# Kernel tuning notes

Hardware: AMD Instinct MI355X
Metric: run time of the kernel (lower is better)

The kernel has to match this reference:

```python
import jax, jax.numpy as jnp
import numpy as np

N = 8192        # nodes
D_IN = 512      # input features
H = 256         # hidden (GAT out_features)
D_OUT = 16      # output classes
K = 16          # num clusters/classes
LRELU_SLOPE = 0.2
MASK_FILL = -9e15
EDGE_P = 0.002  # sparsity of random adjacency


def setup_inputs() -> dict:
    key = jax.random.key(0)
    k1, k2, k3, k4, k5, k6 = jax.random.split(key, 6)
    x = jax.random.normal(k1, (N, D_IN), dtype=jnp.float32)
    # binary adjacency with self loops (module only tests adj > 0; support reused as propagation matrix)
    adj = (jax.random.uniform(k2, (N, N)) < EDGE_P).astype(jnp.float32)
    adj = jnp.maximum(adj, jnp.eye(N, dtype=jnp.float32))
    C_a = jax.random.normal(k3, (K, H), dtype=jnp.float32)
    # learned parameters (xavier-ish scale)
    W = jax.random.normal(k4, (D_IN, H), dtype=jnp.float32) * (1.414 * (2.0 / (D_IN + H)) ** 0.5)
    a = jax.random.normal(k5, (2 * H, 1), dtype=jnp.float32) * (1.414 * (2.0 / (2 * H + 1)) ** 0.5)
    W_gcn = jax.random.normal(k6, (H, D_OUT), dtype=jnp.float32)
    return {"x": x, "adj": adj, "C_a": C_a, "W": W, "a": a, "W_gcn": W_gcn}


def _clust_score(Z, C):
    # score[n,k] = exp(-||Z_n - C_k||) normalized over k (beta = 1)
    d = jnp.sqrt(((Z[:, None, :] - C[None, :, :]) ** 2).sum(-1))  # [N,K]
    s = jnp.exp(-d) + 1e-10
    return s / s.sum(axis=1, keepdims=True)


def reference(x, adj, C_a, W, a, W_gcn):
    h = W.shape[1]
    # --- GAT layer ---
    Wh = x @ W                                   # [N,H]
    Wh1 = Wh @ a[:h, :]                          # [N,1]
    Wh2 = Wh @ a[h:, :]                          # [N,1]
    e = jax.nn.leaky_relu(Wh1 + Wh2.T, LRELU_SLOPE)   # [N,N]
    att = jax.nn.softmax(jnp.where(adj > 0, e, MASK_FILL), axis=1)
    Z_0 = att @ Wh                               # h_prime, [N,H]
    gatoutput = jax.nn.elu(Z_0)
    # --- cluster score on detached Z_0 (update=False path) ---
    score = _clust_score(jax.lax.stop_gradient(Z_0), C_a)
    # --- GCN layer (B_1 = I, so Z_1 = F_1) ---
    F_1 = jax.nn.relu(adj @ (gatoutput @ W_gcn))  # [N,D_OUT]
    output = F_1
    Z_1 = F_1
    return (output, Z_1, Z_0, score)
```

## Files before the change

kernel.cpp:

```cpp
#include <hip/hip_runtime.h>
#include <hip/hip_bf16.h>

#define N_NODES 8192
#define D_IN    512
#define H       256
#define D_OUT   16
#define K_CL    16
#define MAXN    96

#define OUT_OFF 0
#define Z1_OFF  131072
#define Z0_OFF  262144
#define SC_OFF  2359296

typedef unsigned int   u32;
typedef unsigned short u16;
typedef __attribute__((ext_vector_type(8))) short bf16x8;
typedef __attribute__((ext_vector_type(4))) float f32x4;

__device__ __forceinline__ float load_in(const void* p, int bf, size_t idx) {
    if (bf) { u32 w = ((const u16*)p)[idx]; return __uint_as_float(w << 16); }
    return ((const float*)p)[idx];
}
__device__ __forceinline__ void store_out(void* p, int bf, size_t idx, float v) {
    if (bf) ((__hip_bfloat16*)p)[idx] = __float2bfloat16(v);
    else    ((float*)p)[idx] = v;
}

__global__ void k_detect(const u32* __restrict__ adjw, int* __restrict__ flag) {
    int t = blockIdx.x * 256 + threadIdx.x;
    int hit = 0;
    #pragma unroll 4
    for (int i = 0; i < 16; i++)
        if (adjw[(size_t)t + (size_t)i * 65536] == 0x00003F80u) hit = 1;
    if (hit) atomicOr(flag, 1);
}

__global__ void k_prep_small(const void* av, const void* C_a, const void* Wgcn,
                             const int* __restrict__ flag,
                             float* a_f, float* Ca_f, float* Wg_f) {
    int bf = *flag;
    int i = blockIdx.x * 256 + threadIdx.x;
    if (i < 512)        a_f[i]         = load_in(av,   bf, i);
    else if (i < 4608)  Ca_f[i - 512]  = load_in(C_a,  bf, i - 512);
    else if (i < 8704)  Wg_f[i - 4608] = load_in(Wgcn, bf, i - 4608);
}

__global__ void k_prep_wt(const void* __restrict__ wraw,
                          const int* __restrict__ flag, u16* __restrict__ Wt) {
    int bf = *flag;
    int idx = blockIdx.x * 256 + threadIdx.x;
    int h = idx >> 9, k = idx & 511;
    float v = load_in(wraw, bf, (size_t)k * H + h);
    __hip_bfloat16 b = __float2bfloat16(v);
    Wt[(size_t)h * D_IN + k] = *(u16*)&b;
}

__global__ __launch_bounds__(256) void k_gemm_wh(
    const void* __restrict__ xraw, const void* __restrict__ wraw,
    const u16* __restrict__ Wt,
    const int* __restrict__ flag, float* __restrict__ Wh)
{
    int bf = *flag;
    __shared__ float xs[32][68];
    __shared__ float ws_[32][68];
    int tid = threadIdx.x;
    int bm = blockIdx.x >> 2, bn = blockIdx.x & 3;
    int m0 = bm * 64, n0 = bn * 64;

    if (bf) {
        int wave = tid >> 6, lane = tid & 63;
        int wr = wave >> 1, wc = wave & 1;
        int r0 = m0 + wr * 32, c0 = n0 + wc * 32;
        int lr = lane & 15, lk = lane >> 4;
        const u16* xp = (const u16*)xraw;
        const u16* a0p = xp + (size_t)(r0 + lr)      * D_IN + lk * 8;
        const u16* a1p = xp + (size_t)(r0 + 16 + lr) * D_IN + lk * 8;
        const u16* b0p = Wt + (size_t)(c0 + lr)      * D_IN + lk * 8;
        const u16* b1p = Wt + (size_t)(c0 + 16 + lr) * D_IN + lk * 8;
        f32x4 acc[2][2] = {};
        #pragma unroll 4
        for (int k0 = 0; k0 < D_IN; k0 += 32) {
            bf16x8 a0 = *(const bf16x8*)(a0p + k0);
            bf16x8 a1 = *(const bf16x8*)(a1p + k0);
            bf16x8 b0 = *(const bf16x8*)(b0p + k0);
            bf16x8 b1 = *(const bf16x8*)(b1p + k0);
            acc[0][0] = __builtin_amdgcn_mfma_f32_16x16x32_bf16(a0, b0, acc[0][0], 0, 0, 0);
            acc[0][1] = __builtin_amdgcn_mfma_f32_16x16x32_bf16(a0, b1, acc[0][1], 0, 0, 0);
            acc[1][0] = __builtin_amdgcn_mfma_f32_16x16x32_bf16(a1, b0, acc[1][0], 0, 0, 0);
            acc[1][1] = __builtin_amdgcn_mfma_f32_16x16x32_bf16(a1, b1, acc[1][1], 0, 0, 0);
        }
        #pragma unroll
        for (int i = 0; i < 2; i++) {
            #pragma unroll
            for (int reg = 0; reg < 4; reg++) {
                int r = r0 + 16 * i + 4 * lk + reg;
                Wh[(size_t)r * H + c0 + lr]      = acc[i][0][reg];
                Wh[(size_t)r * H + c0 + 16 + lr] = acc[i][1][reg];
            }
        }
        return;
    }

    int tx = tid & 15, ty = tid >> 4;
    float acc[4][4] = {};
    for (int k0 = 0; k0 < D_IN; k0 += 32) {
        {
            int r = tid >> 2, kq = (tid & 3) * 8;
            size_t base = (size_t)(m0 + r) * D_IN + k0 + kq;
            float4 f0 = *(const float4*)((const float*)xraw + base);
            float4 f1 = *(const float4*)((const float*)xraw + base + 4);
            xs[kq + 0][r] = f0.x; xs[kq + 1][r] = f0.y;
            xs[kq + 2][r] = f0.z; xs[kq + 3][r] = f0.w;
            xs[kq + 4][r] = f1.x; xs[kq + 5][r] = f1.y;
            xs[kq + 6][r] = f1.z; xs[kq + 7][r] = f1.w;
        }
        {
            int kk = tid >> 3, n8 = (tid & 7) * 8;
            size_t base = (size_t)(k0 + kk) * H + n0 + n8;
            float4 f0 = *(const float4*)((const float*)wraw + base);
            float4 f1 = *(const float4*)((const float*)wraw + base + 4);
            ws_[kk][n8+0]=f0.x; ws_[kk][n8+1]=f0.y; ws_[kk][n8+2]=f0.z; ws_[kk][n8+3]=f0.w;
            ws_[kk][n8+4]=f1.x; ws_[kk][n8+5]=f1.y; ws_[kk][n8+6]=f1.z; ws_[kk][n8+7]=f1.w;
        }
        __syncthreads();
        #pragma unroll
        for (int kk = 0; kk < 32; kk++) {
            float4 a4 = *(const float4*)&xs[kk][ty * 4];
            float4 b4 = *(const float4*)&ws_[kk][tx * 4];
            float a[4] = {a4.x, a4.y, a4.z, a4.w};
            float b[4] = {b4.x, b4.y, b4.z, b4.w};
            #pragma unroll
            for (int i = 0; i < 4; i++)
                #pragma unroll
                for (int j = 0; j < 4; j++)
                    acc[i][j] += a[i] * b[j];
        }
        __syncthreads();
    }
    #pragma unroll
    for (int i = 0; i < 4; i++) {
        float4 o = {acc[i][0], acc[i][1], acc[i][2], acc[i][3]};
        *(float4*)&Wh[(size_t)(m0 + ty*4 + i) * H + n0 + tx*4] = o;
    }
}

__global__ __launch_bounds__(256) void k_wh12(
    const float* __restrict__ Wh, const float* __restrict__ a_f,
    float* __restrict__ Wh1, float* __restrict__ Wh2)
{
    int tid = threadIdx.x;
    int wave = tid >> 6, lane = tid & 63;
    int n = blockIdx.x * 4 + wave;
    float4 v  = *(const float4*)(Wh + (size_t)n * H + lane * 4);
    float4 a1 = *(const float4*)(a_f + lane * 4);
    float4 a2 = *(const float4*)(a_f + H + lane * 4);
    float s1 = v.x*a1.x + v.y*a1.y + v.z*a1.z + v.w*a1.w;
    float s2 = v.x*a2.x + v.y*a2.y + v.z*a2.z + v.w*a2.w;
    #pragma unroll
    for (int off = 32; off; off >>= 1) {
        s1 += __shfl_xor(s1, off);
        s2 += __shfl_xor(s2, off);
    }
    if (lane == 0) { Wh1[n] = s1; Wh2[n] = s2; }
}

__global__ __launch_bounds__(256) void k_gat_row(
    const void* __restrict__ adjraw, const int* __restrict__ flag,
    const float* __restrict__ Wh,
    const float* __restrict__ Wh1, const float* __restrict__ Wh2,
    const float* __restrict__ Ca_f, const float* __restrict__ Wg_f,
    float* __restrict__ Gf,
    int* __restrict__ nbr_cnt, u16* __restrict__ nbr_idx,
    void* __restrict__ dout)
{
    const int n = blockIdx.x;
    const int tid = threadIdx.x;
    const int bf = *flag;
    __shared__ int   s_cnt;
    __shared__ int   s_idx[MAXN];
    __shared__ float s_att[MAXN];
    __shared__ float s_z[H];
    __shared__ float s_g[H];
    __shared__ float s_red[256];
    __shared__ float s_sc[16];

    if (tid == 0) s_cnt = 0;
    __syncthreads();

    if (bf) {
        const u16* arow = (const u16*)adjraw + (size_t)n * N_NODES;
        #pragma unroll
        for (int it = 0; it < 4; it++) {
            int base = it * 2048 + tid * 8;
            uint4 raw = *(const uint4*)(arow + base);
            u32 rw[4] = {raw.x, raw.y, raw.z, raw.w};
            #pragma unroll
            for (int q = 0; q < 4; q++) {
                #pragma unroll
                for (int hh = 0; hh < 2; hh++) {
                    u32 u = (rw[q] >> (16 * hh)) & 0xFFFFu;
                    if (__uint_as_float(u << 16) > 0.f) {
                        int p = atomicAdd(&s_cnt, 1);
                        if (p < MAXN) s_idx[p] = base + q * 2 + hh;
                    }
                }
            }
        }
    } else {
        const float* arow = (const float*)adjraw + (size_t)n * N_NODES;
        #pragma unroll
        for (int it = 0; it < 8; it++) {
            int base = it * 1024 + tid * 4;
            float4 v = *(const float4*)(arow + base);
            float vv[4] = {v.x, v.y, v.z, v.w};
            #pragma unroll
            for (int q = 0; q < 4; q++) {
                if (vv[q] > 0.f) {
                    int p = atomicAdd(&s_cnt, 1);
                    if (p < MAXN) s_idx[p] = base + q;
                }
            }
        }
    }
    __syncthreads();
    const int cnt = min(s_cnt, MAXN);
    if (tid == 0) nbr_cnt[n] = cnt;
    if (tid < cnt) nbr_idx[(size_t)n * MAXN + tid] = (u16)s_idx[tid];

    float e = 0.f;
    if (tid < cnt) {
        float v = Wh1[n] + Wh2[s_idx[tid]];
        e = v > 0.f ? v : 0.2f * v;
    }
    int lane = tid & 63, wv = tid >> 6;
    float vmax = (tid < cnt) ? e : -3e38f;
    #pragma unroll
    for (int off = 32; off; off >>= 1) vmax = fmaxf(vmax, __shfl_xor(vmax, off));
    if (lane == 0) s_red[wv] = vmax;
    __syncthreads();
    float m = fmaxf(fmaxf(s_red[0], s_red[1]), fmaxf(s_red[2], s_red[3]));
    float wexp = (tid < cnt) ? expf(e - m) : 0.f;
    float ssum = wexp;
    #pragma unroll
    for (int off = 32; off; off >>= 1) ssum += __shfl_xor(ssum, off);
    if (lane == 0) s_red[8 + wv] = ssum;
    __syncthreads();
    float denom = s_red[8] + s_red[9] + s_red[10] + s_red[11];
    if (tid < cnt) s_att[tid] = wexp / denom;
    __syncthreads();

    float acc = 0.f;
    {
        int t = 0;
        for (; t + 4 <= cnt; t += 4) {
            int i0 = s_idx[t], i1 = s_idx[t+1], i2 = s_idx[t+2], i3 = s_idx[t+3];
            float w0 = s_att[t], w1 = s_att[t+1], w2 = s_att[t+2], w3 = s_att[t+3];
            float x0 = Wh[(size_t)i0 * H + tid];
            float x1 = Wh[(size_t)i1 * H + tid];
            float x2 = Wh[(size_t)i2 * H + tid];
            float x3 = Wh[(size_t)i3 * H + tid];
            acc += w0 * x0; acc += w1 * x1; acc += w2 * x2; acc += w3 * x3;
        }
        for (; t < cnt; t++)
            acc += s_att[t] * Wh[(size_t)s_idx[t] * H + tid];
    }
    s_z[tid] = acc;
    store_out(dout, bf, (size_t)Z0_OFF + (size_t)n * H + tid, acc);
    s_g[tid] = acc > 0.f ? acc : expf(acc) - 1.f;
    __syncthreads();

    {
        int k = tid & 15, hb = (tid >> 4) * 16;
        float p = 0.f;
        #pragma unroll
        for (int i = 0; i < 16; i++) {
            float d = s_z[hb + i] - Ca_f[(size_t)k * H + hb + i];
            p += d * d;
        }
        s_red[tid] = p;
    }
    __syncthreads();
    if (tid < 16) {
        float d2 = 0.f;
        #pragma unroll
        for (int q = 0; q < 16; q++) d2 += s_red[q * 16 + tid];
        s_sc[tid] = expf(-sqrtf(d2)) + 1e-10f;
    }
    __syncthreads();
    if (tid < 16) {
        float tot = 0.f;
        #pragma unroll
        for (int q = 0; q < 16; q++) tot += s_sc[q];
        store_out(dout, bf, (size_t)SC_OFF + (size_t)n * K_CL + tid, s_sc[tid] / tot);
    }
    __syncthreads();

    {
        int o = tid & 15, hb = (tid >> 4) * 16;
        float p = 0.f;
        #pragma unroll
        for (int i = 0; i < 16; i++)
            p += s_g[hb + i] * Wg_f[(size_t)(hb + i) * D_OUT + o];
        s_red[tid] = p;
    }
    __syncthreads();
    if (tid < 16) {
        float g2 = 0.f;
        #pragma unroll
        for (int q = 0; q < 16; q++) g2 += s_red[q * 16 + tid];
        Gf[(size_t)n * D_OUT + tid] = g2;
    }
}

__global__ __launch_bounds__(256) void k_f1(
    const int* __restrict__ nbr_cnt, const u16* __restrict__ nbr_idx,
    const float* __restrict__ Gf, const int* __restrict__ flag,
    void* __restrict__ dout)
{
    int tid = threadIdx.x;
    int bf = *flag;
    int r = tid >> 4, o = tid & 15;
    int n = blockIdx.x * 16 + r;
    int cnt = nbr_cnt[n];
    const u16* idx = nbr_idx + (size_t)n * MAXN;
    float acc = 0.f;
    int t = 0;
    for (; t + 4 <= cnt; t += 4) {
        int i0 = idx[t], i1 = idx[t+1], i2 = idx[t+2], i3 = idx[t+3];
        float g0 = Gf[(size_t)i0 * D_OUT + o];
        float g1 = Gf[(size_t)i1 * D_OUT + o];
        float g2 = Gf[(size_t)i2 * D_OUT + o];
        float g3 = Gf[(size_t)i3 * D_OUT + o];
        acc += g0; acc += g1; acc += g2; acc += g3;
    }
    for (; t < cnt; t++)
        acc += Gf[(size_t)idx[t] * D_OUT + o];
    acc = fmaxf(acc, 0.f);
    store_out(dout, bf, (size_t)OUT_OFF + (size_t)n * D_OUT + o, acc);
    store_out(dout, bf, (size_t)Z1_OFF  + (size_t)n * D_OUT + o, acc);
}

extern "C" void kernel_launch(void* const* d_in, const int* in_sizes, int n_in,
                              void* d_out, int out_size, void* d_ws, size_t ws_size,
                              hipStream_t stream) {
    const void* x    = d_in[0];
    const void* adj  = d_in[1];
    const void* C_a  = d_in[2];
    const void* W    = d_in[3];
    const void* av   = d_in[4];
    const void* Wgcn = d_in[5];

    char* wsp = (char*)d_ws;
    int*   flag = (int*)wsp;                   wsp += 256;
    float* Wh   = (float*)wsp;                 wsp += (size_t)N_NODES * H * 4;
    float* Wh1  = (float*)wsp;                 wsp += (size_t)N_NODES * 4;
    float* Wh2  = (float*)wsp;                 wsp += (size_t)N_NODES * 4;
    float* Gf   = (float*)wsp;                 wsp += (size_t)N_NODES * D_OUT * 4;
    int*   ncnt = (int*)wsp;                   wsp += (size_t)N_NODES * 4;
    u16*   nidx = (u16*)wsp;                   wsp += (size_t)N_NODES * MAXN * 2;
    float* a_f  = (float*)wsp;                 wsp += 2 * H * 4;
    float* Ca_f = (float*)wsp;                 wsp += (size_t)K_CL * H * 4;
    float* Wg_f = (float*)wsp;                 wsp += (size_t)H * D_OUT * 4;
    u16*   Wt   = (u16*)wsp;                   wsp += (size_t)H * D_IN * 2;

    hipMemsetAsync(flag, 0, sizeof(int), stream);
    k_detect    <<<256, 256, 0, stream>>>((const u32*)adj, flag);
    k_prep_small<<<34, 256, 0, stream>>>(av, C_a, Wgcn, flag, a_f, Ca_f, Wg_f);
    k_prep_wt   <<<512, 256, 0, stream>>>(W, flag, Wt);
    k_gemm_wh   <<<512, 256, 0, stream>>>(x, W, Wt, flag, Wh);
    k_wh12      <<<N_NODES / 4, 256, 0, stream>>>(Wh, a_f, Wh1, Wh2);
    k_gat_row   <<<N_NODES, 256, 0, stream>>>(adj, flag, Wh, Wh1, Wh2, Ca_f, Wg_f,
                                              Gf, ncnt, nidx, d_out);
    k_f1        <<<N_NODES / 16, 256, 0, stream>>>(ncnt, nidx, Gf, flag, d_out);
}
```

Before: 443.9 us.

## Restructure GAT row kernel to one wave per node, drop detect kernel

Replaces the separate dtype-detect kernel and memset with an inline check of the first adjacency word. The GAT row kernel now processes four nodes per block, one per wave, so shuffles replace block-wide barriers, and it skips empty adjacency chunks quickly. In bf16 mode it gathers neighbour features from a new bf16 copy of Wh written by the GEMM. The W transpose now goes through a shared-memory tile. The inline detection assumes adj[0][0] is a self-loop of 1.0, which may not hold for every input.

After: 494.9 us. 1.11x slower.

```diff
diff --git a/kernel.cpp b/kernel.cpp
--- a/kernel.cpp
+++ b/kernel.cpp
@@ -26,42 +26,52 @@
     if (bf) ((__hip_bfloat16*)p)[idx] = __float2bfloat16(v);
     else    ((float*)p)[idx] = v;
 }
-
-__global__ void k_detect(const u32* __restrict__ adjw, int* __restrict__ flag) {
-    int t = blockIdx.x * 256 + threadIdx.x;
-    int hit = 0;
-    #pragma unroll 4
-    for (int i = 0; i < 16; i++)
-        if (adjw[(size_t)t + (size_t)i * 65536] == 0x00003F80u) hit = 1;
-    if (hit) atomicOr(flag, 1);
-}
+__device__ __forceinline__ int detect_bf(const void* adj) {
+    return ((const u32*)adj)[0] != 0x3F800000u;
+}
+__device__ __forceinline__ float bf2f(u32 h) { return __uint_as_float(h << 16); }
 
 __global__ void k_prep_small(const void* av, const void* C_a, const void* Wgcn,
-                             const int* __restrict__ flag,
+                             const void* __restrict__ adj,
                              float* a_f, float* Ca_f, float* Wg_f) {
-    int bf = *flag;
+    int bf = detect_bf(adj);
     int i = blockIdx.x * 256 + threadIdx.x;
     if (i < 512)        a_f[i]         = load_in(av,   bf, i);
     else if (i < 4608)  Ca_f[i - 512]  = load_in(C_a,  bf, i - 512);
     else if (i < 8704)  Wg_f[i - 4608] = load_in(Wgcn, bf, i - 4608);
 }
 
-__global__ void k_prep_wt(const void* __restrict__ wraw,
-                          const int* __restrict__ flag, u16* __restrict__ Wt) {
-    int bf = *flag;
-    int idx = blockIdx.x * 256 + threadIdx.x;
-    int h = idx >> 9, k = idx & 511;
-    float v = load_in(wraw, bf, (size_t)k * H + h);
-    __hip_bfloat16 b = __float2bfloat16(v);
-    Wt[(size_t)h * D_IN + k] = *(u16*)&b;
+__global__ __launch_bounds__(256) void k_prep_wt(
+    const void* __restrict__ wraw, const void* __restrict__ adj,
+    u16* __restrict__ Wt)
+{
+    int bf = detect_bf(adj);
+    __shared__ float tile[64][65];
+    int b = blockIdx.x;
+    int k0 = (b >> 2) * 64, h0 = (b & 3) * 64;
+    int tid = threadIdx.x;
+    int hh = tid & 63, kk = tid >> 6;
+    #pragma unroll
+    for (int p = 0; p < 16; p++) {
+        int k = kk * 16 + p;
+        tile[k][hh] = load_in(wraw, bf, (size_t)(k0 + k) * H + h0 + hh);
+    }
+    __syncthreads();
+    int kc = tid & 63, hr = tid >> 6;
+    #pragma unroll
+    for (int p = 0; p < 16; p++) {
+        int h = hr * 16 + p;
+        __hip_bfloat16 bb = __float2bfloat16(tile[kc][h]);
+        Wt[(size_t)(h0 + h) * D_IN + k0 + kc] = *(u16*)&bb;
+    }
 }
 
 __global__ __launch_bounds__(256) void k_gemm_wh(
     const void* __restrict__ xraw, const void* __restrict__ wraw,
-    const u16* __restrict__ Wt,
-    const int* __restrict__ flag, float* __restrict__ Wh)
-{
-    int bf = *flag;
+    const u16* __restrict__ Wt, const void* __restrict__ adj,
+    float* __restrict__ Wh, u16* __restrict__ Whb)
+{
+    int bf = detect_bf(adj);
     __shared__ float xs[32][68];
     __shared__ float ws_[32][68];
     int tid = threadIdx.x;
@@ -95,8 +105,12 @@
             #pragma unroll
             for (int reg = 0; reg < 4; reg++) {
                 int r = r0 + 16 * i + 4 * lk + reg;
-                Wh[(size_t)r * H + c0 + lr]      = acc[i][0][reg];
-                Wh[(size_t)r * H + c0 + 16 + lr] = acc[i][1][reg];
+                float v0 = acc[i][0][reg], v1 = acc[i][1][reg];
+                Wh[(size_t)r * H + c0 + lr]      = v0;
+                Wh[(size_t)r * H + c0 + 16 + lr] = v1;
+                __hip_bfloat16 h0 = __float2bfloat16(v0), h1 = __float2bfloat16(v1);
+                Whb[(size_t)r * H + c0 + lr]      = *(u16*)&h0;
+                Whb[(size_t)r * H + c0 + 16 + lr] = *(u16*)&h1;
             }
         }
         return;
@@ -166,160 +180,160 @@
 }
 
 __global__ __launch_bounds__(256) void k_gat_row(
-    const void* __restrict__ adjraw, const int* __restrict__ flag,
-    const float* __restrict__ Wh,
+    const void* __restrict__ adjraw,
+    const float* __restrict__ Wh, const u16* __restrict__ Whb,
     const float* __restrict__ Wh1, const float* __restrict__ Wh2,
     const float* __restrict__ Ca_f, const float* __restrict__ Wg_f,
     float* __restrict__ Gf,
     int* __restrict__ nbr_cnt, u16* __restrict__ nbr_idx,
     void* __restrict__ dout)
 {
-    const int n = blockIdx.x;
     const int tid = threadIdx.x;
-    const int bf = *flag;
-    __shared__ int   s_cnt;
-    __shared__ int   s_idx[MAXN];
-    __shared__ float s_att[MAXN];
-    __shared__ float s_z[H];
-    __shared__ float s_g[H];
-    __shared__ float s_red[256];
-    __shared__ float s_sc[16];
-
-    if (tid == 0) s_cnt = 0;
-    __syncthreads();
+    const int w = tid >> 6, lane = tid & 63;
+    const int n = blockIdx.x * 4 + w;
+    const int bf = detect_bf(adjraw);
+
+    __shared__ int   s_cnt[4];
+    __shared__ int   s_idx[4][MAXN];
+    __shared__ float s_z[4][H];
+    __shared__ float s_g[4][H];
+
+    if (lane == 0) s_cnt[w] = 0;
 
     if (bf) {
         const u16* arow = (const u16*)adjraw + (size_t)n * N_NODES;
         #pragma unroll
-        for (int it = 0; it < 4; it++) {
-            int base = it * 2048 + tid * 8;
+        for (int it = 0; it < 16; it++) {
+            int base = it * 512 + lane * 8;
             uint4 raw = *(const uint4*)(arow + base);
-            u32 rw[4] = {raw.x, raw.y, raw.z, raw.w};
-            #pragma unroll
-            for (int q = 0; q < 4; q++) {
+            if (raw.x | raw.y | raw.z | raw.w) {
+                u32 rw[4] = {raw.x, raw.y, raw.z, raw.w};
                 #pragma unroll
-                for (int hh = 0; hh < 2; hh++) {
-                    u32 u = (rw[q] >> (16 * hh)) & 0xFFFFu;
-                    if (__uint_as_float(u << 16) > 0.f) {
-                        int p = atomicAdd(&s_cnt, 1);
-                        if (p < MAXN) s_idx[p] = base + q * 2 + hh;
+                for (int q = 0; q < 4; q++)
+                    #pragma unroll
+                    for (int hh = 0; hh < 2; hh++) {
+                        u32 u = (rw[q] >> (16 * hh)) & 0xFFFFu;
+                        if (bf2f(u) > 0.f) {
+                            int p = atomicAdd(&s_cnt[w], 1);
+                            if (p < MAXN) s_idx[w][p] = base + q * 2 + hh;
+                        }
                     }
-                }
             }
         }
     } else {
         const float* arow = (const float*)adjraw + (size_t)n * N_NODES;
         #pragma unroll
-        for (int it = 0; it < 8; it++) {
-            int base = it * 1024 + tid * 4;
+        for (int it = 0; it < 32; it++) {
+            int base = it * 256 + lane * 4;
             float4 v = *(const float4*)(arow + base);
-            float vv[4] = {v.x, v.y, v.z, v.w};
-            #pragma unroll
-            for (int q = 0; q < 4; q++) {
-                if (vv[q] > 0.f) {
-                    int p = atomicAdd(&s_cnt, 1);
-                    if (p < MAXN) s_idx[p] = base + q;
-                }
+            if (v.x + v.y + v.z + v.w > 0.f) {
+                float vv[4] = {v.x, v.y, v.z, v.w};
+                #pragma unroll
+                for (int q = 0; q < 4; q++)
+                    if (vv[q] > 0.f) {
+                        int p = atomicAdd(&s_cnt[w], 1);
+                        if (p < MAXN) s_idx[w][p] = base + q;
+                    }
             }
         }
     }
     __syncthreads();
-    const int cnt = min(s_cnt, MAXN);
-    if (tid == 0) nbr_cnt[n] = cnt;
-    if (tid < cnt) nbr_idx[(size_t)n * MAXN + tid] = (u16)s_idx[tid];
-
-    float e = 0.f;
-    if (tid < cnt) {
-        float v = Wh1[n] + Wh2[s_idx[tid]];
-        e = v > 0.f ? v : 0.2f * v;
-    }
-    int lane = tid & 63, wv = tid >> 6;
-    float vmax = (tid < cnt) ? e : -3e38f;
-    #pragma unroll
-    for (int off = 32; off; off >>= 1) vmax = fmaxf(vmax, __shfl_xor(vmax, off));
-    if (lane == 0) s_red[wv] = vmax;
+    const int cnt = min(s_cnt[w], MAXN);
+    if (lane == 0) nbr_cnt[n] = cnt;
+    int i1 = 0, i2 = 0;
+    if (lane < cnt)      i1 = s_idx[w][lane];
+    if (lane + 64 < cnt) i2 = s_idx[w][lane + 64];
+    if (lane < cnt)      nbr_idx[(size_t)n * MAXN + lane]      = (u16)i1;
+    if (lane + 64 < cnt) nbr_idx[(size_t)n * MAXN + lane + 64] = (u16)i2;
+
+    const float wh1n = Wh1[n];
+    float e1 = -3e38f, e2 = -3e38f;
+    if (lane < cnt)      { float v = wh1n + Wh2[i1]; e1 = v > 0.f ? v : 0.2f * v; }
+    if (lane + 64 < cnt) { float v = wh1n + Wh2[i2]; e2 = v > 0.f ? v : 0.2f * v; }
+    float m = fmaxf(e1, e2);
+    #pragma unroll
+    for (int off = 32; off; off >>= 1) m = fmaxf(m, __shfl_xor(m, off));
+    float x1 = (lane < cnt)      ? expf(e1 - m) : 0.f;
+    float x2 = (lane + 64 < cnt) ? expf(e2 - m) : 0.f;
+    float ssum = x1 + x2;
+    #pragma unroll
+    for (int off = 32; off; off >>= 1) ssum += __shfl_xor(ssum, off);
+    float inv = 1.f / ssum;
+    float at1 = x1 * inv, at2 = x2 * inv;
+
+    const int c4 = lane * 4;
+    float az[4] = {0.f, 0.f, 0.f, 0.f};
+    if (bf) {
+        for (int t = 0; t < cnt; t++) {
+            int   it_ = __shfl((t < 64) ? i1 : i2, t & 63);
+            float wt_ = __shfl((t < 64) ? at1 : at2, t & 63);
+            uint2 r = *(const uint2*)(Whb + (size_t)it_ * H + c4);
+            az[0] += wt_ * bf2f(r.x & 0xFFFFu);
+            az[1] += wt_ * bf2f(r.x >> 16);
+            az[2] += wt_ * bf2f(r.y & 0xFFFFu);
+            az[3] += wt_ * bf2f(r.y >> 16);
+        }
+    } else {
+        for (int t = 0; t < cnt; t++) {
+            int   it_ = __shfl((t < 64) ? i1 : i2, t & 63);
+            float wt_ = __shfl((t < 64) ? at1 : at2, t & 63);
+            float4 v = *(const float4*)(Wh + (size_t)it_ * H + c4);
+            az[0] += wt_ * v.x; az[1] += wt_ * v.y;
+            az[2] += wt_ * v.z; az[3] += wt_ * v.w;
+        }
+    }
+    #pragma unroll
+    for (int q = 0; q < 4; q++) {
+        float z = az[q];
+        store_out(dout, bf, (size_t)Z0_OFF + (size_t)n * H + c4 + q, z);
+        s_z[w][c4 + q] = z;
+        s_g[w][c4 + q] = z > 0.f ? z : expf(z) - 1.f;
+    }
     __syncthreads();
-    float m = fmaxf(fmaxf(s_red[0], s_red[1]), fmaxf(s_red[2], s_red[3]));
-    float wexp = (tid < cnt) ? expf(e - m) : 0.f;
-    float ssum = wexp;
-    #pragma unroll
-    for (int off = 32; off; off >>= 1) ssum += __shfl_xor(ssum, off);
-    if (lane == 0) s_red[8 + wv] = ssum;
-    __syncthreads();
-    float denom = s_red[8] + s_red[9] + s_red[10] + s_red[11];
-    if (tid < cnt) s_att[tid] = wexp / denom;
-    __syncthreads();
-
-    float acc = 0.f;
+
     {
-        int t = 0;
-        for (; t + 4 <= cnt; t += 4) {
-            int i0 = s_idx[t], i1 = s_idx[t+1], i2 = s_idx[t+2], i3 = s_idx[t+3];
-            float w0 = s_att[t], w1 = s_att[t+1], w2 = s_att[t+2], w3 = s_att[t+3];
-            float x0 = Wh[(size_t)i0 * H + tid];
-            float x1 = Wh[(size_t)i1 * H + tid];
-            float x2 = Wh[(size_t)i2 * H + tid];
-            float x3 = Wh[(size_t)i3 * H + tid];
-            acc += w0 * x0; acc += w1 * x1; acc += w2 * x2; acc += w3 * x3;
-        }
-        for (; t < cnt; t++)
-            acc += s_att[t] * Wh[(size_t)s_idx[t] * H + tid];
-    }
-    s_z[tid] = acc;
-    store_out(dout, bf, (size_t)Z0_OFF + (size_t)n * H + tid, acc);
-    s_g[tid] = acc > 0.f ? acc : expf(acc) - 1.f;
-    __syncthreads();
+        int k = lane & 15, g = lane >> 4;
+        const float* cz = &s_z[w][0];
+        const float* ck = Ca_f + (size_t)k * H;
+        float d2 = 0.f;
+        #pragma unroll 8
+        for (int i = 0; i < 64; i++) {
+            int ch = g * 64 + ((i + g * 16) & 63);
+            float d = cz[ch] - ck[ch];
+            d2 += d * d;
+        }
+        d2 += __shfl_xor(d2, 16);
+        d2 += __shfl_xor(d2, 32);
+        float sc = expf(-sqrtf(d2)) + 1e-10f;
+        float tot = sc;
+        tot += __shfl_xor(tot, 1); tot += __shfl_xor(tot, 2);
+        tot += __shfl_xor(tot, 4); tot += __shfl_xor(tot, 8);
+        if (lane < 16)
+            store_out(dout, bf, (size_t)SC_OFF + (size_t)n * K_CL + lane, sc / tot);
+    }
 
     {
-        int k = tid & 15, hb = (tid >> 4) * 16;
+        int o = lane & 15, g = lane >> 4;
+        const float* cg = &s_g[w][0];
         float p = 0.f;
-        #pragma unroll
-        for (int i = 0; i < 16; i++) {
-            float d = s_z[hb + i] - Ca_f[(size_t)k * H + hb + i];
-            p += d * d;
-        }
-        s_red[tid] = p;
-    }
-    __syncthreads();
-    if (tid < 16) {
-        float d2 = 0.f;
-        #pragma unroll
-        for (int q = 0; q < 16; q++) d2 += s_red[q * 16 + tid];
-        s_sc[tid] = expf(-sqrtf(d2)) + 1e-10f;
-    }
-    __syncthreads();
-    if (tid < 16) {
-        float tot = 0.f;
-        #pragma unroll
-        for (int q = 0; q < 16; q++) tot += s_sc[q];
-        store_out(dout, bf, (size_t)SC_OFF + (size_t)n * K_CL + tid, s_sc[tid] / tot);
-    }
-    __syncthreads();
-
-    {
-        int o = tid & 15, hb = (tid >> 4) * 16;
-        float p = 0.f;
-        #pragma unroll
-        for (int i = 0; i < 16; i++)
-            p += s_g[hb + i] * Wg_f[(size_t)(hb + i) * D_OUT + o];
-        s_red[tid] = p;
-    }
-    __syncthreads();
-    if (tid < 16) {
-        float g2 = 0.f;
-        #pragma unroll
-        for (int q = 0; q < 16; q++) g2 += s_red[q * 16 + tid];
-        Gf[(size_t)n * D_OUT + tid] = g2;
+        #pragma unroll 8
+        for (int i = 0; i < 64; i++) {
+            int ch = g * 64 + ((i + g * 16) & 63);
+            p += cg[ch] * Wg_f[(size_t)ch * D_OUT + o];
+        }
+        p += __shfl_xor(p, 16);
+        p += __shfl_xor(p, 32);
+        if (lane < 16) Gf[(size_t)n * D_OUT + lane] = p;
     }
 }
 
 __global__ __launch_bounds__(256) void k_f1(
     const int* __restrict__ nbr_cnt, const u16* __restrict__ nbr_idx,
-    const float* __restrict__ Gf, const int* __restrict__ flag,
+    const float* __restrict__ Gf, const void* __restrict__ adj,
     void* __restrict__ dout)
 {
     int tid = threadIdx.x;
-    int bf = *flag;
+    int bf = detect_bf(adj);
     int r = tid >> 4, o = tid & 15;
     int n = blockIdx.x * 16 + r;
     int cnt = nbr_cnt[n];
@@ -352,8 +366,8 @@
     const void* Wgcn = d_in[5];
 
     char* wsp = (char*)d_ws;
-    int*   flag = (int*)wsp;                   wsp += 256;
     float* Wh   = (float*)wsp;                 wsp += (size_t)N_NODES * H * 4;
+    u16*   Whb  = (u16*)wsp;                   wsp += (size_t)N_NODES * H * 2;
     float* Wh1  = (float*)wsp;                 wsp += (size_t)N_NODES * 4;
     float* Wh2  = (float*)wsp;                 wsp += (size_t)N_NODES * 4;
     float* Gf   = (float*)wsp;                 wsp += (size_t)N_NODES * D_OUT * 4;
@@ -364,13 +378,11 @@
     float* Wg_f = (float*)wsp;                 wsp += (size_t)H * D_OUT * 4;
     u16*   Wt   = (u16*)wsp;                   wsp += (size_t)H * D_IN * 2;
 
-    hipMemsetAsync(flag, 0, sizeof(int), stream);
-    k_detect    <<<256, 256, 0, stream>>>((const u32*)adj, flag);
-    k_prep_small<<<34, 256, 0, stream>>>(av, C_a, Wgcn, flag, a_f, Ca_f, Wg_f);
-    k_prep_wt   <<<512, 256, 0, stream>>>(W, flag, Wt);
-    k_gemm_wh   <<<512, 256, 0, stream>>>(x, W, Wt, flag, Wh);
+    k_prep_small<<<34, 256, 0, stream>>>(av, C_a, Wgcn, adj, a_f, Ca_f, Wg_f);
+    k_prep_wt   <<<32, 256, 0, stream>>>(W, adj, Wt);
+    k_gemm_wh   <<<512, 256, 0, stream>>>(x, W, Wt, adj, Wh, Whb);
     k_wh12      <<<N_NODES / 4, 256, 0, stream>>>(Wh, a_f, Wh1, Wh2);
-    k_gat_row   <<<N_NODES, 256, 0, stream>>>(adj, flag, Wh, Wh1, Wh2, Ca_f, Wg_f,
-                                              Gf, ncnt, nidx, d_out);
-    k_f1        <<<N_NODES / 16, 256, 0, stream>>>(ncnt, nidx, Gf, flag, d_out);
-}
+    k_gat_row   <<<N_NODES / 4, 256, 0, stream>>>(adj, Wh, Whb, Wh1, Wh2, Ca_f, Wg_f,
+                                                  Gf, ncnt, nidx, d_out);
+    k_f1        <<<N_NODES / 16, 256, 0, stream>>>(ncnt, nidx, Gf, adj, d_out);
+}
```
